# Kernel optimization log

Hardware: AMD Instinct MI355X
Metric: run time of the kernel (lower is better)

## Reference

```python
import jax, jax.numpy as jnp
import numpy as np

LEAKY_SLOPE = 0.2


def _sample_ball(key, n, dim, radius):
    # uniform in unit ball: normalize gaussian, scale by U^(1/dim)
    k1, k2 = jax.random.split(key)
    g = jax.random.normal(k1, (n, dim), dtype=jnp.float32)
    g = g / jnp.linalg.norm(g, axis=-1, keepdims=True)
    r = jax.random.uniform(k2, (n, 1), dtype=jnp.float32) ** (1.0 / dim)
    return radius * g * r


def setup_inputs() -> dict:
    key = jax.random.key(0)
    ks = jax.random.split(key, 8)
    B, N, D, K = 16, 4096, 3, 4096
    IN, H1, H2, OUT = K + K * D, 1024, 512, 256
    point_cloud = jax.random.normal(ks[0], (B, N, D), dtype=jnp.float32) * 0.3
    basis = _sample_ball(ks[1], K, D, 1.0)
    s = 0.02
    W1 = jax.random.normal(ks[2], (IN, H1), dtype=jnp.float32) * s
    b1 = jnp.zeros((H1,), dtype=jnp.float32)
    W2 = jax.random.normal(ks[3], (H1, H2), dtype=jnp.float32) * s
    b2 = jnp.zeros((H2,), dtype=jnp.float32)
    W3 = jax.random.normal(ks[4], (H2, OUT), dtype=jnp.float32) * s
    b3 = jnp.zeros((OUT,), dtype=jnp.float32)
    return {"point_cloud": point_cloud, "basis": basis,
            "W1": W1, "b1": b1, "W2": W2, "b2": b2, "W3": W3, "b3": b3}


def _bps_encode(pc, basis):
    # pc: [B,N,3], basis: [K,3]
    # squared cdist via gemm expansion (avoids [B,K,N,3] broadcast)
    pn = jnp.sum(pc * pc, axis=-1)                     # [B,N]
    bn = jnp.sum(basis * basis, axis=-1)               # [K]
    cross = jnp.einsum('kd,bnd->bkn', basis, pc)       # [B,K,N]
    d2 = bn[None, :, None] + pn[:, None, :] - 2.0 * cross
    idx = jnp.argmin(d2, axis=-1)                      # [B,K]
    nearest = jnp.take_along_axis(pc, idx[..., None], axis=1)  # [B,K,3]
    deltas = nearest - basis[None, :, :]               # [B,K,3]
    dists = jnp.linalg.norm(deltas, axis=-1)           # [B,K]
    return dists, deltas


def reference(point_cloud, basis, W1, b1, W2, b2, W3, b3):
    B = point_cloud.shape[0]
    dists, deltas = _bps_encode(point_cloud, basis)
    bps_feature = jnp.concatenate([dists, deltas.reshape(B, -1)], axis=-1)  # [B, K+3K]
    h = bps_feature @ W1 + b1
    h = jnp.where(h >= 0, h, LEAKY_SLOPE * h)
    h = h @ W2 + b2
    h = jnp.where(h >= 0, h, LEAKY_SLOPE * h)
    global_feature = h @ W3 + b3
    return (global_feature, bps_feature[:, None, :])
```

## Files before the change

### kernel.cpp

```cpp
#include <hip/hip_runtime.h>

#define LEAKY_SLOPE 0.2f

constexpr int B_   = 16;
constexpr int N_   = 4096;
constexpr int K_   = 4096;
constexpr int IN_  = 16384;
constexpr int H1_  = 1024;
constexpr int H2_  = 512;
constexpr int OUT_ = 256;

constexpr int NCH = 64;
constexpr int NPC = N_ / NCH;
constexpr int KPT = 8;
constexpr int KTB = 256 * KPT;

constexpr int GCH = 128;

__global__ __launch_bounds__(256) void enc_partial(
    const float* __restrict__ pc, const float* __restrict__ basis,
    float* __restrict__ chunkminf)
{
#pragma clang fp contract(off)
    __shared__ float4 pts[NPC + 1];
    const int kt = blockIdx.x;
    const int b  = blockIdx.y;
    const int c  = blockIdx.z;
    const int n0 = c * NPC;

    if (threadIdx.x < NPC) {
        const float* pp = pc + ((size_t)b * N_ + n0 + threadIdx.x) * 3;
        float x = pp[0], y = pp[1], z = pp[2];
        pts[threadIdx.x] = make_float4(x, y, z, (x * x + y * y) + z * z);
    }
    if (threadIdx.x == 0) pts[NPC] = make_float4(0.f, 0.f, 0.f, 0.f);
    __syncthreads();

    const int k0 = kt * KTB + (int)threadIdx.x;
    float nbx[KPT], nby[KPT], nbz[KPT], best[KPT];
#pragma unroll
    for (int q = 0; q < KPT; ++q) {
        int k = k0 + q * 256;
        nbx[q] = -2.0f * basis[k * 3 + 0];
        nby[q] = -2.0f * basis[k * 3 + 1];
        nbz[q] = -2.0f * basis[k * 3 + 2];
        best[q] = 3.4028235e38f;
    }

    float4 pcur = pts[0];
#pragma unroll 4
    for (int n = 0; n < NPC; ++n) {
        float4 pnext = pts[n + 1];
#pragma unroll
        for (int q = 0; q < KPT; ++q) {
            float e2 = __builtin_fmaf(nbx[q], pcur.x,
                        __builtin_fmaf(nby[q], pcur.y,
                         __builtin_fmaf(nbz[q], pcur.z, pcur.w)));
            best[q] = __builtin_fminf(best[q], e2);
        }
        pcur = pnext;
    }

    float* dst = chunkminf + ((size_t)(c * B_ + b)) * K_;
#pragma unroll
    for (int q = 0; q < KPT; ++q)
        dst[k0 + q * 256] = best[q];
}

__global__ __launch_bounds__(256) void enc_reduce_finish(
    const float* __restrict__ pc, const float* __restrict__ basis,
    const float* __restrict__ chunkminf,
    float* __restrict__ bps_out)
{
#pragma clang fp contract(off)
    const int t = blockIdx.x * 256 + (int)threadIdx.x;
    const int b = t >> 12;
    const int k = t & (K_ - 1);

    float m = 3.4028235e38f;
    int   cb = 0;
#pragma unroll 8
    for (int c = 0; c < NCH; ++c) {
        float v = chunkminf[((size_t)(c * B_ + b)) * K_ + k];
        if (v < m) { m = v; cb = c; }
    }

    const float bx0 = basis[k * 3 + 0];
    const float by0 = basis[k * 3 + 1];
    const float bz0 = basis[k * 3 + 2];
    const float nbx = -2.0f * bx0;
    const float nby = -2.0f * by0;
    const float nbz = -2.0f * bz0;

    const float4* pch = (const float4*)(pc + ((size_t)b * N_ + cb * NPC) * 3);
    float mm = 3.4028235e38f;
    float px = 0.f, py = 0.f, pz = 0.f;
#pragma unroll 4
    for (int g = 0; g < NPC / 4; ++g) {
        float4 q0 = pch[3 * g + 0];
        float4 q1 = pch[3 * g + 1];
        float4 q2 = pch[3 * g + 2];
        float xs[4] = { q0.x, q0.w, q1.z, q2.y };
        float ys[4] = { q0.y, q1.x, q1.w, q2.z };
        float zs[4] = { q0.z, q1.y, q2.x, q2.w };
#pragma unroll
        for (int j = 0; j < 4; ++j) {
            float x = xs[j], y = ys[j], z = zs[j];
            float pw = (x * x + y * y) + z * z;
            float e2 = __builtin_fmaf(nbx, x,
                        __builtin_fmaf(nby, y,
                         __builtin_fmaf(nbz, z, pw)));
            if (e2 < mm) { mm = e2; px = x; py = y; pz = z; }
        }
    }

    float dx = px - bx0;
    float dy = py - by0;
    float dz = pz - bz0;
    float dist = sqrtf((dx * dx + dy * dy) + dz * dz);

    float* row = bps_out + (size_t)b * IN_;
    row[k]              = dist;
    row[K_ + 3 * k + 0] = dx;
    row[K_ + 3 * k + 1] = dy;
    row[K_ + 3 * k + 2] = dz;
}

template<int ILEN, int NCOLS>
__global__ __launch_bounds__(256) void gemm1(
    const float* __restrict__ A, const float* __restrict__ W,
    float* __restrict__ part)
{
    __shared__ float red[4][64][33];
    const int lane = (int)threadIdx.x & 63;
    const int w    = __builtin_amdgcn_readfirstlane((int)threadIdx.x >> 6);
    const int j0   = blockIdx.x * 128 + lane * 2;
    const int i0   = blockIdx.y * ILEN + w * (ILEN / 4);

    float2 acc[16];
#pragma unroll
    for (int r = 0; r < 16; ++r) acc[r] = make_float2(0.f, 0.f);

#pragma unroll 4
    for (int i = i0; i < i0 + ILEN / 4; ++i) {
        float2 wv = *(const float2*)(W + (size_t)i * NCOLS + j0);
#pragma unroll
        for (int r = 0; r < 16; ++r) {
            float a = A[(size_t)r * IN_ + i];
            acc[r].x = __builtin_fmaf(a, wv.x, acc[r].x);
            acc[r].y = __builtin_fmaf(a, wv.y, acc[r].y);
        }
    }

#pragma unroll
    for (int r = 0; r < 16; ++r) {
        red[w][lane][2 * r]     = acc[r].x;
        red[w][lane][2 * r + 1] = acc[r].y;
    }
    __syncthreads();

    float* base = part + (size_t)blockIdx.y * 16 * NCOLS + blockIdx.x * 128 + lane * 2;
    const int b0 = w * 4;
#pragma unroll
    for (int b = b0; b < b0 + 4; ++b) {
        float sx = 0.f, sy = 0.f;
#pragma unroll
        for (int ww = 0; ww < 4; ++ww) {
            sx += red[ww][lane][2 * b];
            sy += red[ww][lane][2 * b + 1];
        }
        *(float2*)(base + (size_t)b * NCOLS) = make_float2(sx, sy);
    }
}

__global__ __launch_bounds__(256) void reduce_act1(
    const float* __restrict__ part, const float* __restrict__ bias,
    float* __restrict__ outT)
{
    const int p = blockIdx.x * 256 + (int)threadIdx.x;
    float s = 0.0f;
#pragma unroll 8
    for (int c = 0; c < GCH; ++c) s += part[(size_t)c * (16 * H1_) + p];
    const int col = p & (H1_ - 1);
    const int b   = p >> 10;
    s += bias[col];
    s = fmaxf(s, LEAKY_SLOPE * s);
    outT[(size_t)col * 16 + b] = s;
}

template<int KDIM, int NCOLS>
__global__ __launch_bounds__(256) void gemm_mid(
    const float* __restrict__ AT, const float* __restrict__ W,
    float* __restrict__ part)
{
    __shared__ float red[4][64][17];
    const int lane = (int)threadIdx.x & 63;
    const int w    = __builtin_amdgcn_readfirstlane((int)threadIdx.x >> 6);
    const int cb   = blockIdx.x;
    const int s    = blockIdx.y;
    const int j    = cb * 64 + lane;
    constexpr int KS = KDIM / 8;
    constexpr int KW = KS / 4;
    const int i0 = s * KS + w * KW;

    float acc[16];
#pragma unroll
    for (int r = 0; r < 16; ++r) acc[r] = 0.0f;

#pragma unroll 4
    for (int i = i0; i < i0 + KW; ++i) {
        float wv = W[(size_t)i * NCOLS + j];
        const float4* Ar = (const float4*)(AT + (size_t)i * 16);
        float4 q0 = Ar[0], q1 = Ar[1], q2 = Ar[2], q3 = Ar[3];
        acc[0]  = __builtin_fmaf(q0.x, wv, acc[0]);
        acc[1]  = __builtin_fmaf(q0.y, wv, acc[1]);
        acc[2]  = __builtin_fmaf(q0.z, wv, acc[2]);
        acc[3]  = __builtin_fmaf(q0.w, wv, acc[3]);
        acc[4]  = __builtin_fmaf(q1.x, wv, acc[4]);
        acc[5]  = __builtin_fmaf(q1.y, wv, acc[5]);
        acc[6]  = __builtin_fmaf(q1.z, wv, acc[6]);
        acc[7]  = __builtin_fmaf(q1.w, wv, acc[7]);
        acc[8]  = __builtin_fmaf(q2.x, wv, acc[8]);
        acc[9]  = __builtin_fmaf(q2.y, wv, acc[9]);
        acc[10] = __builtin_fmaf(q2.z, wv, acc[10]);
        acc[11] = __builtin_fmaf(q2.w, wv, acc[11]);
        acc[12] = __builtin_fmaf(q3.x, wv, acc[12]);
        acc[13] = __builtin_fmaf(q3.y, wv, acc[13]);
        acc[14] = __builtin_fmaf(q3.z, wv, acc[14]);
        acc[15] = __builtin_fmaf(q3.w, wv, acc[15]);
    }

#pragma unroll
    for (int r = 0; r < 16; ++r) red[w][lane][r] = acc[r];
    __syncthreads();

#pragma unroll
    for (int q = 0; q < 4; ++q) {
        int p  = (int)threadIdx.x * 4 + q;
        int cl = p >> 4;
        int bt = p & 15;
        float ssum = 0.0f;
#pragma unroll
        for (int ww = 0; ww < 4; ++ww) ssum += red[ww][cl][bt];
        part[((size_t)s * NCOLS + cb * 64 + cl) * 16 + bt] = ssum;
    }
}

template<int KDIM, int NCOLS>
__global__ __launch_bounds__(256) void gemm_last(
    const float* __restrict__ h2part, const float* __restrict__ b2,
    const float* __restrict__ W, float* __restrict__ part)
{
    __shared__ float aT[64][20];
    __shared__ float red[4][64][17];
    const int lane = (int)threadIdx.x & 63;
    const int w    = __builtin_amdgcn_readfirstlane((int)threadIdx.x >> 6);
    const int cb   = blockIdx.x;
    const int s    = blockIdx.y;
    constexpr int KS = KDIM / 8;

    {
        const int il  = (int)threadIdx.x >> 2;
        const int btq = ((int)threadIdx.x & 3) * 4;
        const int i   = s * KS + il;
        float4 sum = make_float4(0.f, 0.f, 0.f, 0.f);
#pragma unroll
        for (int sl = 0; sl < 8; ++sl) {
            const float4 v = *(const float4*)(h2part +
                ((size_t)sl * H2_ + i) * 16 + btq);
            sum.x += v.x; sum.y += v.y; sum.z += v.z; sum.w += v.w;
        }
        const float bb = b2[i];
        sum.x += bb; sum.y += bb; sum.z += bb; sum.w += bb;
        sum.x = fmaxf(sum.x, LEAKY_SLOPE * sum.x);
        sum.y = fmaxf(sum.y, LEAKY_SLOPE * sum.y);
        sum.z = fmaxf(sum.z, LEAKY_SLOPE * sum.z);
        sum.w = fmaxf(sum.w, LEAKY_SLOPE * sum.w);
        *(float4*)&aT[il][btq] = sum;
    }
    __syncthreads();

    const int j  = cb * 64 + lane;
    const int i0 = w * 16;
    float acc[16];
#pragma unroll
    for (int r = 0; r < 16; ++r) acc[r] = 0.0f;

#pragma unroll 4
    for (int il = i0; il < i0 + 16; ++il) {
        float wv = W[((size_t)(s * KS + il)) * NCOLS + j];
        float4 q0 = *(const float4*)&aT[il][0];
        float4 q1 = *(const float4*)&aT[il][4];
        float4 q2 = *(const float4*)&aT[il][8];
        float4 q3 = *(const float4*)&aT[il][12];
        acc[0]  = __builtin_fmaf(q0.x, wv, acc[0]);
        acc[1]  = __builtin_fmaf(q0.y, wv, acc[1]);
        acc[2]  = __builtin_fmaf(q0.z, wv, acc[2]);
        acc[3]  = __builtin_fmaf(q0.w, wv, acc[3]);
        acc[4]  = __builtin_fmaf(q1.x, wv, acc[4]);
        acc[5]  = __builtin_fmaf(q1.y, wv, acc[5]);
        acc[6]  = __builtin_fmaf(q1.z, wv, acc[6]);
        acc[7]  = __builtin_fmaf(q1.w, wv, acc[7]);
        acc[8]  = __builtin_fmaf(q2.x, wv, acc[8]);
        acc[9]  = __builtin_fmaf(q2.y, wv, acc[9]);
        acc[10] = __builtin_fmaf(q2.z, wv, acc[10]);
        acc[11] = __builtin_fmaf(q2.w, wv, acc[11]);
        acc[12] = __builtin_fmaf(q3.x, wv, acc[12]);
        acc[13] = __builtin_fmaf(q3.y, wv, acc[13]);
        acc[14] = __builtin_fmaf(q3.z, wv, acc[14]);
        acc[15] = __builtin_fmaf(q3.w, wv, acc[15]);
    }

#pragma unroll
    for (int r = 0; r < 16; ++r) red[w][lane][r] = acc[r];
    __syncthreads();

#pragma unroll
    for (int q = 0; q < 4; ++q) {
        int p  = (int)threadIdx.x * 4 + q;
        int cl = p >> 4;
        int bt = p & 15;
        float ssum = 0.0f;
#pragma unroll
        for (int ww = 0; ww < 4; ++ww) ssum += red[ww][cl][bt];
        part[((size_t)s * NCOLS + cb * 64 + cl) * 16 + bt] = ssum;
    }
}

__global__ __launch_bounds__(256) void out_final(
    const float* __restrict__ h3part, const float* __restrict__ b3,
    float* __restrict__ out)
{
    const int t   = blockIdx.x * 256 + (int)threadIdx.x;
    const int col = t >> 4;
    const int bt  = t & 15;
    float s = b3[col];
#pragma unroll
    for (int sl = 0; sl < 8; ++sl)
        s += h3part[((size_t)sl * OUT_ + col) * 16 + bt];
    out[(size_t)bt * OUT_ + col] = s;
}

extern "C" void kernel_launch(void* const* d_in, const int* in_sizes, int n_in,
                              void* d_out, int out_size, void* d_ws, size_t ws_size,
                              hipStream_t stream)
{
    const float* pc    = (const float*)d_in[0];
    const float* basis = (const float*)d_in[1];
    const float* W1    = (const float*)d_in[2];
    const float* b1    = (const float*)d_in[3];
    const float* W2    = (const float*)d_in[4];
    const float* b2    = (const float*)d_in[5];
    const float* W3    = (const float*)d_in[6];
    const float* b3    = (const float*)d_in[7];

    float* out   = (float*)d_out;
    float* gfeat = out;
    float* bps   = out + B_ * OUT_;

    char* ws = (char*)d_ws;
    float* chunkminf = (float*)ws;
    float* partial = (float*)(ws + (size_t)16 * 1024 * 1024);
    float* h1T     = (float*)(ws + (size_t)24 * 1024 * 1024);
    float* h2part  = (float*)(ws + (size_t)24 * 1024 * 1024 + 64 * 1024);
    float* h3part  = (float*)(ws + (size_t)24 * 1024 * 1024 + 320 * 1024);

    enc_partial<<<dim3(K_ / KTB, B_, NCH), 256, 0, stream>>>(pc, basis, chunkminf);
    enc_reduce_finish<<<(B_ * K_) / 256, 256, 0, stream>>>(pc, basis, chunkminf, bps);
    gemm1<128, H1_><<<dim3(8, GCH), 256, 0, stream>>>(bps, W1, partial);
    reduce_act1<<<(H1_ * 16) / 256, 256, 0, stream>>>(partial, b1, h1T);
    gemm_mid<1024, H2_><<<dim3(8, 8), 256, 0, stream>>>(h1T, W2, h2part);
    gemm_last<512, OUT_><<<dim3(4, 8), 256, 0, stream>>>(h2part, b2, W3, h3part);
    out_final<<<16, 256, 0, stream>>>(h3part, b3, gfeat);
}
```

Before: 166.8 us.

## Merge final GEMM with output reduction and pair points in encoder loop

```diff
diff --git a/kernel.cpp b/kernel.cpp
--- a/kernel.cpp
+++ b/kernel.cpp
@@ -22,7 +22,7 @@
     float* __restrict__ chunkminf)
 {
 #pragma clang fp contract(off)
-    __shared__ float4 pts[NPC + 1];
+    __shared__ float4 pts[NPC + 2];
     const int kt = blockIdx.x;
     const int b  = blockIdx.y;
     const int c  = blockIdx.z;
@@ -33,7 +33,8 @@
         float x = pp[0], y = pp[1], z = pp[2];
         pts[threadIdx.x] = make_float4(x, y, z, (x * x + y * y) + z * z);
     }
-    if (threadIdx.x == 0) pts[NPC] = make_float4(0.f, 0.f, 0.f, 0.f);
+    if (threadIdx.x < 2)
+        pts[NPC + threadIdx.x] = make_float4(0.f, 0.f, 0.f, 0.f);
     __syncthreads();
 
     const int k0 = kt * KTB + (int)threadIdx.x;
@@ -47,18 +48,23 @@
         best[q] = 3.4028235e38f;
     }
 
-    float4 pcur = pts[0];
-#pragma unroll 4
-    for (int n = 0; n < NPC; ++n) {
-        float4 pnext = pts[n + 1];
+    float4 pa = pts[0];
+    float4 pb = pts[1];
+#pragma unroll 2
+    for (int n = 0; n < NPC; n += 2) {
+        float4 pc2 = pts[n + 2];
+        float4 pd  = pts[n + 3];
 #pragma unroll
         for (int q = 0; q < KPT; ++q) {
-            float e2 = __builtin_fmaf(nbx[q], pcur.x,
-                        __builtin_fmaf(nby[q], pcur.y,
-                         __builtin_fmaf(nbz[q], pcur.z, pcur.w)));
-            best[q] = __builtin_fminf(best[q], e2);
-        }
-        pcur = pnext;
+            float ea = __builtin_fmaf(nbx[q], pa.x,
+                        __builtin_fmaf(nby[q], pa.y,
+                         __builtin_fmaf(nbz[q], pa.z, pa.w)));
+            float eb = __builtin_fmaf(nbx[q], pb.x,
+                        __builtin_fmaf(nby[q], pb.y,
+                         __builtin_fmaf(nbz[q], pb.z, pb.w)));
+            best[q] = __builtin_fminf(best[q], __builtin_fminf(ea, eb));
+        }
+        pa = pc2; pb = pd;
     }
 
     float* dst = chunkminf + ((size_t)(c * B_ + b)) * K_;
@@ -249,28 +255,29 @@
 template<int KDIM, int NCOLS>
 __global__ __launch_bounds__(256) void gemm_last(
     const float* __restrict__ h2part, const float* __restrict__ b2,
-    const float* __restrict__ W, float* __restrict__ part)
-{
-    __shared__ float aT[64][20];
+    const float* __restrict__ W, const float* __restrict__ b3,
+    float* __restrict__ outp)
+{
+    __shared__ float aT[KDIM][20];
     __shared__ float red[4][64][17];
-    const int lane = (int)threadIdx.x & 63;
-    const int w    = __builtin_amdgcn_readfirstlane((int)threadIdx.x >> 6);
-    const int cb   = blockIdx.x;
-    const int s    = blockIdx.y;
-    constexpr int KS = KDIM / 8;
-
-    {
-        const int il  = (int)threadIdx.x >> 2;
-        const int btq = ((int)threadIdx.x & 3) * 4;
-        const int i   = s * KS + il;
+    const int tid  = (int)threadIdx.x;
+    const int lane = tid & 63;
+    const int w    = __builtin_amdgcn_readfirstlane(tid >> 6);
+    const int cb   = (int)blockIdx.x;
+
+#pragma unroll
+    for (int u = 0; u < 8; ++u) {
+        const int item = tid * 8 + u;
+        const int il   = item >> 2;
+        const int btq  = (item & 3) * 4;
         float4 sum = make_float4(0.f, 0.f, 0.f, 0.f);
 #pragma unroll
         for (int sl = 0; sl < 8; ++sl) {
             const float4 v = *(const float4*)(h2part +
-                ((size_t)sl * H2_ + i) * 16 + btq);
+                ((size_t)sl * H2_ + il) * 16 + btq);
             sum.x += v.x; sum.y += v.y; sum.z += v.z; sum.w += v.w;
         }
-        const float bb = b2[i];
+        const float bb = b2[il];
         sum.x += bb; sum.y += bb; sum.z += bb; sum.w += bb;
         sum.x = fmaxf(sum.x, LEAKY_SLOPE * sum.x);
         sum.y = fmaxf(sum.y, LEAKY_SLOPE * sum.y);
@@ -281,14 +288,14 @@
     __syncthreads();
 
     const int j  = cb * 64 + lane;
-    const int i0 = w * 16;
+    const int i0 = w * (KDIM / 4);
     float acc[16];
 #pragma unroll
     for (int r = 0; r < 16; ++r) acc[r] = 0.0f;
 
 #pragma unroll 4
-    for (int il = i0; il < i0 + 16; ++il) {
-        float wv = W[((size_t)(s * KS + il)) * NCOLS + j];
+    for (int il = i0; il < i0 + KDIM / 4; ++il) {
+        float wv = W[(size_t)il * NCOLS + j];
         float4 q0 = *(const float4*)&aT[il][0];
         float4 q1 = *(const float4*)&aT[il][4];
         float4 q2 = *(const float4*)&aT[il][8];
@@ -317,28 +324,15 @@
 
 #pragma unroll
     for (int q = 0; q < 4; ++q) {
-        int p  = (int)threadIdx.x * 4 + q;
+        int p  = tid * 4 + q;
         int cl = p >> 4;
         int bt = p & 15;
-        float ssum = 0.0f;
-#pragma unroll
-        for (int ww = 0; ww < 4; ++ww) ssum += red[ww][cl][bt];
-        part[((size_t)s * NCOLS + cb * 64 + cl) * 16 + bt] = ssum;
-    }
-}
-
-__global__ __launch_bounds__(256) void out_final(
-    const float* __restrict__ h3part, const float* __restrict__ b3,
-    float* __restrict__ out)
-{
-    const int t   = blockIdx.x * 256 + (int)threadIdx.x;
-    const int col = t >> 4;
-    const int bt  = t & 15;
-    float s = b3[col];
-#pragma unroll
-    for (int sl = 0; sl < 8; ++sl)
-        s += h3part[((size_t)sl * OUT_ + col) * 16 + bt];
-    out[(size_t)bt * OUT_ + col] = s;
+        const int col = cb * 64 + cl;
+        float s = b3[col];
+#pragma unroll
+        for (int ww = 0; ww < 4; ++ww) s += red[ww][cl][bt];
+        outp[(size_t)bt * NCOLS + col] = s;
+    }
 }
 
 extern "C" void kernel_launch(void* const* d_in, const int* in_sizes, int n_in,
@@ -363,13 +357,11 @@
     float* partial = (float*)(ws + (size_t)16 * 1024 * 1024);
     float* h1T     = (float*)(ws + (size_t)24 * 1024 * 1024);
     float* h2part  = (float*)(ws + (size_t)24 * 1024 * 1024 + 64 * 1024);
-    float* h3part  = (float*)(ws + (size_t)24 * 1024 * 1024 + 320 * 1024);
 
     enc_partial<<<dim3(K_ / KTB, B_, NCH), 256, 0, stream>>>(pc, basis, chunkminf);
     enc_reduce_finish<<<(B_ * K_) / 256, 256, 0, stream>>>(pc, basis, chunkminf, bps);
     gemm1<128, H1_><<<dim3(8, GCH), 256, 0, stream>>>(bps, W1, partial);
     reduce_act1<<<(H1_ * 16) / 256, 256, 0, stream>>>(partial, b1, h1T);
     gemm_mid<1024, H2_><<<dim3(8, 8), 256, 0, stream>>>(h1T, W2, h2part);
-    gemm_last<512, OUT_><<<dim3(4, 8), 256, 0, stream>>>(h2part, b2, W3, h3part);
-    out_final<<<16, 256, 0, stream>>>(h3part, b3, gfeat);
-}
+    gemm_last<512, OUT_><<<4, 256, 0, stream>>>(h2part, b2, W3, b3, gfeat);
+}
```

Result: slower. 190.1 us (+14.0%).
